# Optimization experiments

Hardware: AMD Instinct MI355X
Metric: run time of the kernel (lower is better)

The kernel has to match this reference:

```python
import jax, jax.numpy as jnp
import numpy as np

K = 20
EPS = 1e-5
SLOPE = 0.2


def knn(x, k=K):
    # x: (B, C, N); returns indices of k nearest neighbors (largest -dist^2), (B, N, k)
    xx = jnp.sum(x * x, axis=1)                      # (B, N)
    inner = jnp.einsum('bcn,bcm->bnm', x, x)         # (B, N, N)
    pd = 2.0 * inner - xx[:, :, None] - xx[:, None, :]  # -squared distance
    _, idx = jax.lax.top_k(pd, k)
    return idx


def graph_feature(x, idx):
    # x: (B, C, N), idx: (B, N, k) -> (B, 2C, N): concat(x, max_k(neighbor) - x)
    feat = jnp.transpose(x, (0, 2, 1))               # (B, N, C)
    nb = jax.vmap(lambda f, i: f[i])(feat, idx)      # (B, N, k, C)
    nb_max = nb.max(axis=2)                          # (B, N, C)
    out = jnp.concatenate([feat, nb_max - feat], axis=-1)  # (B, N, 2C)
    return jnp.transpose(out, (0, 2, 1))


def conv_bn_lrelu(x, W, g, b):
    # 1x1 Conv2d (no bias) on (B,C,N,1) == channel matmul; BN2d training-mode; LeakyReLU
    h = jnp.einsum('oc,bcn->bon', W, x)              # (B, O, N)
    mu = h.mean(axis=(0, 2), keepdims=True)
    var = h.var(axis=(0, 2), keepdims=True)
    h = (h - mu) / jnp.sqrt(var + EPS) * g[None, :, None] + b[None, :, None]
    return jax.nn.leaky_relu(h, SLOPE)


def bn1d_lrelu(h, g, b):
    mu = h.mean(axis=0, keepdims=True)
    var = h.var(axis=0, keepdims=True)
    h = (h - mu) / jnp.sqrt(var + EPS) * g[None, :] + b[None, :]
    return jax.nn.leaky_relu(h, SLOPE)


def forward(x, W1, g1, b1, W2, g2, b2, W3, g3, b3, W4, g4, b4, W5, g5, b5,
            L1, g6, b6, L2, bl2, g7, b7, L3, bl3):
    B = x.shape[0]
    idx = knn(x)                                      # knn on raw xyz
    h = conv_bn_lrelu(x, W1, g1, b1)                  # (B, 64, N)
    x1 = graph_feature(h, idx)                        # (B, 128, N)

    idx = knn(x1)
    h = conv_bn_lrelu(x1, W2, g2, b2)                 # (B, 64, N)
    x2 = graph_feature(h, idx)                        # (B, 128, N)

    idx = knn(x2)
    h = conv_bn_lrelu(x2, W3, g3, b3)                 # (B, 64, N)
    x3 = graph_feature(h, idx)                        # (B, 128, N)

    idx = knn(x3)
    h = conv_bn_lrelu(x3, W4, g4, b4)                 # (B, 128, N)
    x4 = graph_feature(h, idx)                        # (B, 256, N)

    xc = jnp.concatenate([x1, x2, x3, x4], axis=1)    # (B, 640, N)
    h5 = conv_bn_lrelu(xc, W5, g5, b5)                # (B, 1024, N)
    feat = h5.max(axis=1)                             # max over CHANNELS -> (B, N=1024)

    h = bn1d_lrelu(feat @ L1.T, g6, b6)               # (B, 512); dropout=identity (eval)
    h = bn1d_lrelu(h @ L2.T + bl2, g7, b7)            # (B, 256)
    return h @ L3.T + bl3                             # (B, 40)


def setup_inputs() -> dict:
    key = jax.random.key(0)
    ks = jax.random.split(key, 32)
    ki = iter(ks)

    def rn(shape, scale=0.1):
        return jax.random.normal(next(ki), shape, dtype=jnp.float32) * scale

    def bn_params(c):
        return 1.0 + rn((c,)), rn((c,))

    x = jax.random.normal(next(ki), (32, 3, 1024), dtype=jnp.float32)
    W1 = rn((64, 3));    g1, b1 = bn_params(64)
    W2 = rn((64, 128));  g2, b2 = bn_params(64)
    W3 = rn((64, 128));  g3, b3 = bn_params(64)
    W4 = rn((128, 128)); g4, b4 = bn_params(128)
    W5 = rn((1024, 640)); g5, b5 = bn_params(1024)
    L1 = rn((512, 1024)); g6, b6 = bn_params(512)
    L2 = rn((256, 512)); bl2 = rn((256,)); g7, b7 = bn_params(256)
    L3 = rn((40, 256));  bl3 = rn((40,))
    return dict(x=x, W1=W1, g1=g1, b1=b1, W2=W2, g2=g2, b2=b2, W3=W3, g3=g3, b3=b3,
                W4=W4, g4=g4, b4=b4, W5=W5, g5=g5, b5=b5, L1=L1, g6=g6, b6=b6,
                L2=L2, bl2=bl2, g7=g7, b7=b7, L3=L3, bl3=bl3)


def reference(x, W1, g1, b1, W2, g2, b2, W3, g3, b3, W4, g4, b4, W5, g5, b5,
              L1, g6, b6, L2, bl2, g7, b7, L3, bl3):
    return forward(x, W1, g1, b1, W2, g2, b2, W3, g3, b3, W4, g4, b4, W5, g5, b5,
                   L1, g6, b6, L2, bl2, g7, b7, L3, bl3)
```

## Files before the change

kernel.cpp:

```cpp
#include <hip/hip_runtime.h>
#include <cfloat>
#include <cstdint>

#define NB 32
#define NPTS 1024
#define KNN 20
#define RTOT (NB * NPTS)

typedef __attribute__((ext_vector_type(8))) short bf16x8;
typedef __attribute__((ext_vector_type(4))) float f32x4;

__device__ __forceinline__ float lrelu(float v) { return v >= 0.f ? v : 0.2f * v; }

__global__ void k_transpose_x(const float* __restrict__ x, float* __restrict__ xT) {
    int g = blockIdx.x * 256 + threadIdx.x;
    if (g >= NB * 3 * NPTS) return;
    int n = g % NPTS;
    int c = (g / NPTS) % 3;
    int b = g / (3 * NPTS);
    xT[((size_t)b * NPTS + n) * 3 + c] = x[g];
}

__global__ void k_xx(const float* __restrict__ X, int ldx, int C, float* __restrict__ xx) {
    int r = blockIdx.x * 256 + threadIdx.x;
    if (r >= RTOT) return;
    const float* p = X + (size_t)r * ldx;
    float s = 0.f;
    for (int c = 0; c < C; ++c) { float v = p[c]; s += v * v; }
    xx[r] = s;
}

__global__ __launch_bounds__(256) void k_gemm_xwt(
    const float* __restrict__ X, int ldx, int K,
    const float* __restrict__ W,
    float* __restrict__ H, int ldh)
{
    __shared__ float As[16][68];
    __shared__ float Bs[16][68];
    int tid = threadIdx.x;
    int tx = tid & 15, ty = tid >> 4;
    int c0 = blockIdx.x * 64;
    int r0 = blockIdx.y * 64;
    float acc[4][4] = {};
    int lr = tid >> 4, lk = tid & 15;
    for (int k0 = 0; k0 < K; k0 += 16) {
#pragma unroll
        for (int i = 0; i < 4; ++i) {
            int row = lr + i * 16;
            int kk = k0 + lk;
            float av = 0.f, bv = 0.f;
            if (kk < K) {
                av = X[(size_t)(r0 + row) * ldx + kk];
                bv = W[(size_t)(c0 + row) * K + kk];
            }
            As[lk][row] = av;
            Bs[lk][row] = bv;
        }
        __syncthreads();
#pragma unroll
        for (int k = 0; k < 16; ++k) {
            float4 a4 = *(const float4*)&As[k][ty * 4];
            float4 b4 = *(const float4*)&Bs[k][tx * 4];
            float av[4] = {a4.x, a4.y, a4.z, a4.w};
            float bv[4] = {b4.x, b4.y, b4.z, b4.w};
#pragma unroll
            for (int i = 0; i < 4; ++i)
#pragma unroll
                for (int j = 0; j < 4; ++j)
                    acc[i][j] = fmaf(av[i], bv[j], acc[i][j]);
        }
        __syncthreads();
    }
#pragma unroll
    for (int i = 0; i < 4; ++i) {
        float4 v = make_float4(acc[i][0], acc[i][1], acc[i][2], acc[i][3]);
        *(float4*)&H[(size_t)(r0 + ty * 4 + i) * ldh + c0 + tx * 4] = v;
    }
}

__global__ __launch_bounds__(256) void k_pd128(
    const float* __restrict__ X, int ldx, int K,
    const float* __restrict__ xx, float* __restrict__ pd)
{
    __shared__ float As[16][132];
    __shared__ float Bs[16][132];
    int b = blockIdx.z;
    int tid = threadIdx.x;
    int tx = tid & 15, ty = tid >> 4;
    int c0 = blockIdx.x * 128;
    int r0 = blockIdx.y * 128;
    const float* Xb = X + (size_t)b * NPTS * ldx;
    int lk = tid & 15, lr = tid >> 4;
    float acc[8][8] = {};
    for (int k0 = 0; k0 < K; k0 += 16) {
#pragma unroll
        for (int i = 0; i < 8; ++i) {
            int row = lr + i * 16;
            int kk = k0 + lk;
            float av = 0.f, bv = 0.f;
            if (kk < K) {
                av = Xb[(size_t)(r0 + row) * ldx + kk];
                bv = Xb[(size_t)(c0 + row) * ldx + kk];
            }
            As[lk][row] = av;
            Bs[lk][row] = bv;
        }
        __syncthreads();
#pragma unroll
        for (int k = 0; k < 16; ++k) {
            float a[8], bb[8];
            *(float4*)&a[0]  = *(const float4*)&As[k][ty * 4];
            *(float4*)&a[4]  = *(const float4*)&As[k][64 + ty * 4];
            *(float4*)&bb[0] = *(const float4*)&Bs[k][tx * 4];
            *(float4*)&bb[4] = *(const float4*)&Bs[k][64 + tx * 4];
#pragma unroll
            for (int i = 0; i < 8; ++i)
#pragma unroll
                for (int j = 0; j < 8; ++j)
                    acc[i][j] = fmaf(a[i], bb[j], acc[i][j]);
        }
        __syncthreads();
    }
    const float* xxb = xx + (size_t)b * NPTS;
    float* pdb = pd + (size_t)b * NPTS * NPTS;
    float xcA[4], xcB[4];
#pragma unroll
    for (int j = 0; j < 4; ++j) {
        xcA[j] = xxb[c0 + tx * 4 + j];
        xcB[j] = xxb[c0 + 64 + tx * 4 + j];
    }
#pragma unroll
    for (int i = 0; i < 8; ++i) {
        int r = r0 + ((i < 4) ? (ty * 4 + i) : (64 + ty * 4 + i - 4));
        float xr = xxb[r];
        float* orow = &pdb[(size_t)r * NPTS + c0];
        float4 v0, v1;
        v0.x = 2.f * acc[i][0] - xr - xcA[0];
        v0.y = 2.f * acc[i][1] - xr - xcA[1];
        v0.z = 2.f * acc[i][2] - xr - xcA[2];
        v0.w = 2.f * acc[i][3] - xr - xcA[3];
        v1.x = 2.f * acc[i][4] - xr - xcB[0];
        v1.y = 2.f * acc[i][5] - xr - xcB[1];
        v1.z = 2.f * acc[i][6] - xr - xcB[2];
        v1.w = 2.f * acc[i][7] - xr - xcB[3];
        *(float4*)&orow[tx * 4]      = v0;
        *(float4*)&orow[64 + tx * 4] = v1;
    }
}

__global__ __launch_bounds__(256) void k_topk_wave(const float* __restrict__ pd, int* __restrict__ idx) {
    int wid = (blockIdx.x * 256 + threadIdx.x) >> 6;
    int lane = threadIdx.x & 63;
    const float* row = pd + (size_t)wid * NPTS;
    float v[16];
#pragma unroll
    for (int j = 0; j < 16; ++j) v[j] = row[lane + 64 * j];
    float bv = v[0]; int bj = 0;
#pragma unroll
    for (int j = 1; j < 16; ++j) if (v[j] > bv) { bv = v[j]; bj = j; }
    int* out = idx + (size_t)wid * KNN;
    for (int kk = 0; kk < KNN; ++kk) {
        float cv = bv;
        int ci = lane + (bj << 6);
#pragma unroll
        for (int s = 1; s < 64; s <<= 1) {
            float ov = __shfl_xor(cv, s);
            int oi = __shfl_xor(ci, s);
            if (ov > cv || (ov == cv && oi < ci)) { cv = ov; ci = oi; }
        }
        if (lane == 0) out[kk] = ci;
        bool mine = (ci & 63) == lane;
        int jdead = ci >> 6;
#pragma unroll
        for (int j = 0; j < 16; ++j) if (mine && j == jdead) v[j] = -FLT_MAX;
        bv = v[0]; bj = 0;
#pragma unroll
        for (int j = 1; j < 16; ++j) if (v[j] > bv) { bv = v[j]; bj = j; }
    }
}

__device__ __forceinline__ void split2(float x, ushort& h, ushort& l) {
    uint u = __float_as_uint(x);
    uint r = u + 0x7FFFu + ((u >> 16) & 1u);
    ushort hh = (ushort)(r >> 16);
    float hf = __uint_as_float((uint)hh << 16);
    float d = x - hf;
    uint u2 = __float_as_uint(d);
    uint r2 = u2 + 0x7FFFu + ((u2 >> 16) & 1u);
    h = hh;
    l = (ushort)(r2 >> 16);
}

__device__ __forceinline__ uint pack2(ushort a, ushort b) { return (uint)a | ((uint)b << 16); }

__device__ __forceinline__ void stage_split(const float* __restrict__ g,
                                            ushort* __restrict__ dh, ushort* __restrict__ dl) {
    float4 v0 = *(const float4*)(g);
    float4 v1 = *(const float4*)(g + 4);
    float4 v2 = *(const float4*)(g + 8);
    float4 v3 = *(const float4*)(g + 12);
    float xs[16] = {v0.x, v0.y, v0.z, v0.w, v1.x, v1.y, v1.z, v1.w,
                    v2.x, v2.y, v2.z, v2.w, v3.x, v3.y, v3.z, v3.w};
    ushort h[16], l[16];
#pragma unroll
    for (int i = 0; i < 16; ++i) split2(xs[i], h[i], l[i]);
    uint4 H0, H1, L0, L1;
    H0.x = pack2(h[0], h[1]);  H0.y = pack2(h[2], h[3]);
    H0.z = pack2(h[4], h[5]);  H0.w = pack2(h[6], h[7]);
    H1.x = pack2(h[8], h[9]);  H1.y = pack2(h[10], h[11]);
    H1.z = pack2(h[12], h[13]); H1.w = pack2(h[14], h[15]);
    L0.x = pack2(l[0], l[1]);  L0.y = pack2(l[2], l[3]);
    L0.z = pack2(l[4], l[5]);  L0.w = pack2(l[6], l[7]);
    L1.x = pack2(l[8], l[9]);  L1.y = pack2(l[10], l[11]);
    L1.z = pack2(l[12], l[13]); L1.w = pack2(l[14], l[15]);
    *(uint4*)(dh)     = H0;
    *(uint4*)(dh + 8) = H1;
    *(uint4*)(dl)     = L0;
    *(uint4*)(dl + 8) = L1;
}

__global__ void k_split(const float* __restrict__ X, ushort* __restrict__ Xh,
                        ushort* __restrict__ Xl, int n) {
    int g = (blockIdx.x * 256 + threadIdx.x) * 8;
    if (g >= n) return;
    float4 a = *(const float4*)(X + g);
    float4 b = *(const float4*)(X + g + 4);
    float xs[8] = {a.x, a.y, a.z, a.w, b.x, b.y, b.z, b.w};
    ushort h[8], l[8];
#pragma unroll
    for (int i = 0; i < 8; ++i) split2(xs[i], h[i], l[i]);
    uint4 H, L;
    H.x = pack2(h[0], h[1]); H.y = pack2(h[2], h[3]);
    H.z = pack2(h[4], h[5]); H.w = pack2(h[6], h[7]);
    L.x = pack2(l[0], l[1]); L.y = pack2(l[2], l[3]);
    L.z = pack2(l[4], l[5]); L.w = pack2(l[6], l[7]);
    *(uint4*)(Xh + g) = H;
    *(uint4*)(Xl + g) = L;
}

#define LDK 40
__global__ __launch_bounds__(256) void k_gemm5_mfma(
    const float* __restrict__ X, const ushort* __restrict__ Wh, const ushort* __restrict__ Wl,
    float* __restrict__ H, float* __restrict__ sums)
{
    __shared__ __align__(16) ushort sAh[128 * LDK];
    __shared__ __align__(16) ushort sAl[128 * LDK];
    __shared__ __align__(16) ushort sBh[128 * LDK];
    __shared__ __align__(16) ushort sBl[128 * LDK];
    int tid = threadIdx.x;
    int lane = tid & 63, w = tid >> 6;
    int wm = w >> 1, wn = w & 1;
    int bid = blockIdx.x;
    int wg = (bid & 7) * 256 + (bid >> 3);
    int cb = wg & 7, rb = wg >> 3;
    int r0 = rb * 128, c0 = cb * 128;
    int srow = tid >> 1, sk = (tid & 1) * 16;
    int fr = lane & 15;
    int kg = (lane >> 4) << 3;
    f32x4 acc[4][4] = {};
    for (int k0 = 0; k0 < 640; k0 += 32) {
        stage_split(X + (size_t)(r0 + srow) * 640 + k0 + sk,
                    &sAh[srow * LDK + sk], &sAl[srow * LDK + sk]);
        {
            size_t gb = (size_t)(c0 + srow) * 640 + k0 + sk;
            *(uint4*)&sBh[srow * LDK + sk]     = *(const uint4*)(Wh + gb);
            *(uint4*)&sBh[srow * LDK + sk + 8] = *(const uint4*)(Wh + gb + 8);
            *(uint4*)&sBl[srow * LDK + sk]     = *(const uint4*)(Wl + gb);
            *(uint4*)&sBl[srow * LDK + sk + 8] = *(const uint4*)(Wl + gb + 8);
        }
        __syncthreads();
        bf16x8 ah[4], al[4];
#pragma unroll
        for (int mi = 0; mi < 4; ++mi) {
            int rr = wm * 64 + mi * 16 + fr;
            ah[mi] = *(const bf16x8*)&sAh[rr * LDK + kg];
            al[mi] = *(const bf16x8*)&sAl[rr * LDK + kg];
        }
#pragma unroll
        for (int ni = 0; ni < 4; ++ni) {
            int cc = wn * 64 + ni * 16 + fr;
            bf16x8 bh = *(const bf16x8*)&sBh[cc * LDK + kg];
            bf16x8 bl = *(const bf16x8*)&sBl[cc * LDK + kg];
#pragma unroll
            for (int mi = 0; mi < 4; ++mi) {
                acc[mi][ni] = __builtin_amdgcn_mfma_f32_16x16x32_bf16(ah[mi], bh, acc[mi][ni], 0, 0, 0);
                acc[mi][ni] = __builtin_amdgcn_mfma_f32_16x16x32_bf16(ah[mi], bl, acc[mi][ni], 0, 0, 0);
                acc[mi][ni] = __builtin_amdgcn_mfma_f32_16x16x32_bf16(al[mi], bh, acc[mi][ni], 0, 0, 0);
            }
        }
        __syncthreads();
    }
#pragma unroll
    for (int mi = 0; mi < 4; ++mi) {
        int rg = r0 + wm * 64 + mi * 16 + (lane >> 4) * 4;
#pragma unroll
        for (int ni = 0; ni < 4; ++ni) {
            int cg = c0 + wn * 64 + ni * 16 + fr;
#pragma unroll
            for (int r = 0; r < 4; ++r)
                H[(size_t)(rg + r) * 1024 + cg] = acc[mi][ni][r];
        }
    }
    float* csum  = (float*)sAh;
    float* csum2 = csum + 128;
    if (tid < 128) { csum[tid] = 0.f; csum2[tid] = 0.f; }
    __syncthreads();
#pragma unroll
    for (int ni = 0; ni < 4; ++ni) {
        float s = 0.f, s2 = 0.f;
#pragma unroll
        for (int mi = 0; mi < 4; ++mi)
#pragma unroll
            for (int r = 0; r < 4; ++r) { float v = acc[mi][ni][r]; s += v; s2 += v * v; }
        int c = wn * 64 + ni * 16 + fr;
        atomicAdd(&csum[c], s);
        atomicAdd(&csum2[c], s2);
    }
    __syncthreads();
    if (tid < 128) {
        atomicAdd(&sums[c0 + tid], csum[tid]);
        atomicAdd(&sums[1024 + c0 + tid], csum2[tid]);
    }
}

__global__ __launch_bounds__(256) void k_bn_stats(const float* __restrict__ H, int ldh, int O, int R,
                                                  float* __restrict__ sums) {
    int nblk = gridDim.x;
    int rows = (R + nblk - 1) / nblk;
    int r0 = blockIdx.x * rows;
    int r1 = r0 + rows; if (r1 > R) r1 = R;
    int tid = threadIdx.x;
    if (O <= 256) {
        int per = 256 / O;
        int c = tid % O;
        int rOff = tid / O;
        float s = 0.f, s2 = 0.f;
        for (int r = r0 + rOff; r < r1; r += per) {
            float v = H[(size_t)r * ldh + c];
            s += v; s2 += v * v;
        }
        __shared__ float ls[256], ls2[256];
        ls[tid] = s; ls2[tid] = s2;
        __syncthreads();
        for (int st = 128; st >= O; st >>= 1) {
            if (tid < st) { ls[tid] += ls[tid + st]; ls2[tid] += ls2[tid + st]; }
            __syncthreads();
        }
        if (tid < O) {
            atomicAdd(&sums[c], ls[tid]);
            atomicAdd(&sums[O + c], ls2[tid]);
        }
    } else {
        int nc = O / 256;
        float s[4] = {0, 0, 0, 0}, s2[4] = {0, 0, 0, 0};
        for (int r = r0; r < r1; ++r) {
            const float* rowp = H + (size_t)r * ldh;
            for (int i = 0; i < nc; ++i) {
                float v = rowp[tid + i * 256];
                s[i] += v; s2[i] += v * v;
            }
        }
        for (int i = 0; i < nc; ++i) {
            atomicAdd(&sums[tid + i * 256], s[i]);
            atomicAdd(&sums[O + tid + i * 256], s2[i]);
        }
    }
}

__global__ void k_bn_finalize(const float* __restrict__ sums, const float* __restrict__ g,
                              const float* __restrict__ bta, int O, float invR,
                              float* __restrict__ ss) {
    int o = blockIdx.x * 256 + threadIdx.x;
    if (o >= O) return;
    float mu = sums[o] * invR;
    float var = sums[O + o] * invR - mu * mu;
    float sc = g[o] / sqrtf(var + 1e-5f);
    ss[o] = sc;
    ss[O + o] = bta[o] - mu * sc;
}

__global__ __launch_bounds__(256) void k_graph_feature(
    const float* __restrict__ hT, int ldh, int C,
    const int* __restrict__ idx, const float* __restrict__ ss,
    float* __restrict__ out, int ldo, int colOff)
{
    int ppb = 256 / C;
    int p = threadIdx.x / C;
    int c = threadIdx.x % C;
    int r = blockIdx.x * ppb + p;
    int b = r >> 10;
    float sc = ss[c], sh = ss[C + c];
    float self = hT[(size_t)r * ldh + c];
    float vs = lrelu(sc * self + sh);
    const int* ip = idx + (size_t)r * KNN;
    float m = -FLT_MAX;
#pragma unroll 4
    for (int k = 0; k < KNN; ++k) {
        int j = ip[k];
        float hv = hT[((size_t)b * NPTS + j) * ldh + c];
        float v = lrelu(sc * hv + sh);
        m = fmaxf(m, v);
    }
    float* orow = out + (size_t)r * ldo + colOff;
    orow[c] = vs;
    orow[C + c] = m - vs;
}

__global__ __launch_bounds__(256) void k_chanmax(const float* __restrict__ h5,
                                                 const float* __restrict__ ss,
                                                 float* __restrict__ feat) {
    int r = blockIdx.x;
    int tid = threadIdx.x;
    __shared__ float red[256];
    const float* rowp = h5 + (size_t)r * 1024;
    float m = -FLT_MAX;
    for (int o = tid; o < 1024; o += 256) {
        float v = lrelu(ss[o] * rowp[o] + ss[1024 + o]);
        m = fmaxf(m, v);
    }
    red[tid] = m;
    __syncthreads();
    for (int s = 128; s > 0; s >>= 1) {
        if (tid < s) red[tid] = fmaxf(red[tid], red[tid + s]);
        __syncthreads();
    }
    if (tid == 0) feat[r] = red[0];
}

__global__ void k_fc(const float* __restrict__ in, const float* __restrict__ Lw,
                     const float* __restrict__ bias, float* __restrict__ out, int K, int J) {
    int g = blockIdx.x * 256 + threadIdx.x;
    if (g >= 32 * J) return;
    int b = g / J, j = g % J;
    const float* xr = in + (size_t)b * K;
    const float* wr = Lw + (size_t)j * K;
    float acc = 0.f;
    for (int k = 0; k < K; ++k) acc = fmaf(xr[k], wr[k], acc);
    out[g] = bias ? acc + bias[j] : acc;
}

__global__ void k_bn1d(float* __restrict__ h, const float* __restrict__ g,
                       const float* __restrict__ bta, int J) {
    int j = blockIdx.x * 256 + threadIdx.x;
    if (j >= J) return;
    float s = 0.f, s2 = 0.f;
    for (int b = 0; b < 32; ++b) {
        float v = h[b * J + j];
        s += v; s2 += v * v;
    }
    float mu = s / 32.f;
    float var = s2 / 32.f - mu * mu;
    float sc = g[j] / sqrtf(var + 1e-5f);
    float sh = bta[j] - mu * sc;
    for (int b = 0; b < 32; ++b) {
        float v = sc * h[b * J + j] + sh;
        h[b * J + j] = lrelu(v);
    }
}

extern "C" void kernel_launch(void* const* d_in, const int* in_sizes, int n_in,
                              void* d_out, int out_size, void* d_ws, size_t ws_size,
                              hipStream_t stream) {
    const float* x   = (const float*)d_in[0];
    const float* W1  = (const float*)d_in[1];
    const float* g1  = (const float*)d_in[2];
    const float* b1  = (const float*)d_in[3];
    const float* W2  = (const float*)d_in[4];
    const float* g2  = (const float*)d_in[5];
    const float* b2  = (const float*)d_in[6];
    const float* W3  = (const float*)d_in[7];
    const float* g3  = (const float*)d_in[8];
    const float* b3  = (const float*)d_in[9];
    const float* W4  = (const float*)d_in[10];
    const float* g4  = (const float*)d_in[11];
    const float* b4  = (const float*)d_in[12];
    const float* W5  = (const float*)d_in[13];
    const float* g5  = (const float*)d_in[14];
    const float* b5  = (const float*)d_in[15];
    const float* L1  = (const float*)d_in[16];
    const float* g6  = (const float*)d_in[17];
    const float* b6  = (const float*)d_in[18];
    const float* L2  = (const float*)d_in[19];
    const float* bl2 = (const float*)d_in[20];
    const float* g7  = (const float*)d_in[21];
    const float* b7  = (const float*)d_in[22];
    const float* L3  = (const float*)d_in[23];
    const float* bl3 = (const float*)d_in[24];

    float* ws = (float*)d_ws;
    size_t off = 0;
    auto alloc = [&](size_t n) { size_t o = off; off += (n + 63) & ~(size_t)63; return o; };
    float* pd   = ws + alloc((size_t)NB * NPTS * NPTS);
    float* h5   = pd;
    float* xcT  = ws + alloc((size_t)RTOT * 640);
    float* hbuf = ws + alloc((size_t)RTOT * 128);
    float* xT   = ws + alloc((size_t)RTOT * 3);
    float* xxb  = ws + alloc(RTOT);
    float* sums = ws + alloc(2048);
    float* ss   = ws + alloc(2048);
    float* feat = ws + alloc(RTOT);
    float* h1   = ws + alloc(32 * 512);
    float* h2   = ws + alloc(32 * 256);
    int*   idxb = (int*)(ws + alloc((size_t)RTOT * KNN));
    ushort* W5h = (ushort*)(ws + alloc(1024 * 640 / 2));
    ushort* W5l = (ushort*)(ws + alloc(1024 * 640 / 2));

    k_transpose_x<<<(NB * 3 * NPTS + 255) / 256, 256, 0, stream>>>(x, xT);
    k_split<<<(1024 * 640 / 8 + 255) / 256, 256, 0, stream>>>(W5, W5h, W5l, 1024 * 640);

    auto run_knn = [&](const float* X, int ldx, int C) {
        k_xx<<<(RTOT + 255) / 256, 256, 0, stream>>>(X, ldx, C, xxb);
        k_pd128<<<dim3(NPTS / 128, NPTS / 128, NB), 256, 0, stream>>>(X, ldx, C, xxb, pd);
        k_topk_wave<<<RTOT / 4, 256, 0, stream>>>(pd, idxb);
    };
    auto run_conv = [&](const float* X, int ldx, int K, const float* W,
                        const float* g, const float* bta, int O) {
        k_gemm_xwt<<<dim3(O / 64, RTOT / 64), 256, 0, stream>>>(X, ldx, K, W, hbuf, O);
        hipMemsetAsync(sums, 0, 2 * O * sizeof(float), stream);
        k_bn_stats<<<256, 256, 0, stream>>>(hbuf, O, O, RTOT, sums);
        k_bn_finalize<<<(O + 255) / 256, 256, 0, stream>>>(sums, g, bta, O, 1.f / RTOT, ss);
    };
    auto run_gf = [&](int C, int colOff) {
        int ppb = 256 / C;
        k_graph_feature<<<RTOT / ppb, 256, 0, stream>>>(hbuf, C, C, idxb, ss, xcT, 640, colOff);
    };

    run_knn(xT, 3, 3);
    run_conv(xT, 3, 3, W1, g1, b1, 64);
    run_gf(64, 0);

    run_knn(xcT + 0, 640, 128);
    run_conv(xcT + 0, 640, 128, W2, g2, b2, 64);
    run_gf(64, 128);

    run_knn(xcT + 128, 640, 128);
    run_conv(xcT + 128, 640, 128, W3, g3, b3, 64);
    run_gf(64, 256);

    run_knn(xcT + 256, 640, 128);
    run_conv(xcT + 256, 640, 128, W4, g4, b4, 128);
    run_gf(128, 384);

    hipMemsetAsync(sums, 0, 2048 * sizeof(float), stream);
    k_gemm5_mfma<<<2048, 256, 0, stream>>>(xcT, W5h, W5l, h5, sums);
    k_bn_finalize<<<4, 256, 0, stream>>>(sums, g5, b5, 1024, 1.f / RTOT, ss);
    k_chanmax<<<RTOT, 256, 0, stream>>>(h5, ss, feat);

    k_fc<<<(32 * 512 + 255) / 256, 256, 0, stream>>>(feat, L1, nullptr, h1, 1024, 512);
    k_bn1d<<<(512 + 255) / 256, 256, 0, stream>>>(h1, g6, b6, 512);
    k_fc<<<(32 * 256 + 255) / 256, 256, 0, stream>>>(h1, L2, bl2, h2, 512, 256);
    k_bn1d<<<(256 + 255) / 256, 256, 0, stream>>>(h2, g7, b7, 256);
    k_fc<<<(32 * 40 + 255) / 256, 256, 0, stream>>>(h2, L3, bl3, (float*)d_out, 256, 40);
}
```

Before: 1.828 ms.

## Exploit pairwise-distance symmetry: compute upper-triangle tiles and mirror-write transposes

The pairwise distance kernel now launches only the 36 upper-triangular 128x128 tiles per batch, not all 64. Each off-diagonal tile writes both its own block and the transposed block, roughly halving the GEMM work for the distance matrix. The feature dimension also becomes a template parameter so the K loop can be unrolled or specialized. The transposed writes are strided across rows and less coalesced, and fewer blocks means lower parallelism per launch.

```diff
diff --git a/kernel.cpp b/kernel.cpp
--- a/kernel.cpp
+++ b/kernel.cpp
@@ -78,17 +78,20 @@
     }
 }
 
-__global__ __launch_bounds__(256) void k_pd128(
-    const float* __restrict__ X, int ldx, int K,
+template<int K>
+__global__ __launch_bounds__(256) void k_pd_sym(
+    const float* __restrict__ X, int ldx,
     const float* __restrict__ xx, float* __restrict__ pd)
 {
     __shared__ float As[16][132];
     __shared__ float Bs[16][132];
-    int b = blockIdx.z;
+    int b = blockIdx.y;
     int tid = threadIdx.x;
     int tx = tid & 15, ty = tid >> 4;
-    int c0 = blockIdx.x * 128;
-    int r0 = blockIdx.y * 128;
+    int t = blockIdx.x, rb = 0, rem = 8;
+    while (t >= rem) { t -= rem; ++rb; --rem; }
+    int cb = rb + t;
+    int r0 = rb * 128, c0 = cb * 128;
     const float* Xb = X + (size_t)b * NPTS * ldx;
     int lk = tid & 15, lr = tid >> 4;
     float acc[8][8] = {};
@@ -123,28 +126,47 @@
     }
     const float* xxb = xx + (size_t)b * NPTS;
     float* pdb = pd + (size_t)b * NPTS * NPTS;
-    float xcA[4], xcB[4];
-#pragma unroll
-    for (int j = 0; j < 4; ++j) {
-        xcA[j] = xxb[c0 + tx * 4 + j];
-        xcB[j] = xxb[c0 + 64 + tx * 4 + j];
-    }
+    float xc[8];
+#pragma unroll
+    for (int j = 0; j < 8; ++j)
+        xc[j] = xxb[c0 + ((j < 4) ? (tx * 4 + j) : (64 + tx * 4 + j - 4))];
+    float xr[8];
+#pragma unroll
+    for (int i = 0; i < 8; ++i)
+        xr[i] = xxb[r0 + ((i < 4) ? (ty * 4 + i) : (64 + ty * 4 + i - 4))];
 #pragma unroll
     for (int i = 0; i < 8; ++i) {
         int r = r0 + ((i < 4) ? (ty * 4 + i) : (64 + ty * 4 + i - 4));
-        float xr = xxb[r];
         float* orow = &pdb[(size_t)r * NPTS + c0];
         float4 v0, v1;
-        v0.x = 2.f * acc[i][0] - xr - xcA[0];
-        v0.y = 2.f * acc[i][1] - xr - xcA[1];
-        v0.z = 2.f * acc[i][2] - xr - xcA[2];
-        v0.w = 2.f * acc[i][3] - xr - xcA[3];
-        v1.x = 2.f * acc[i][4] - xr - xcB[0];
-        v1.y = 2.f * acc[i][5] - xr - xcB[1];
-        v1.z = 2.f * acc[i][6] - xr - xcB[2];
-        v1.w = 2.f * acc[i][7] - xr - xcB[3];
+        v0.x = 2.f * acc[i][0] - xr[i] - xc[0];
+        v0.y = 2.f * acc[i][1] - xr[i] - xc[1];
+        v0.z = 2.f * acc[i][2] - xr[i] - xc[2];
+        v0.w = 2.f * acc[i][3] - xr[i] - xc[3];
+        v1.x = 2.f * acc[i][4] - xr[i] - xc[4];
+        v1.y = 2.f * acc[i][5] - xr[i] - xc[5];
+        v1.z = 2.f * acc[i][6] - xr[i] - xc[6];
+        v1.w = 2.f * acc[i][7] - xr[i] - xc[7];
         *(float4*)&orow[tx * 4]      = v0;
         *(float4*)&orow[64 + tx * 4] = v1;
+    }
+    if (cb > rb) {
+#pragma unroll
+        for (int j = 0; j < 8; ++j) {
+            int c = c0 + ((j < 4) ? (tx * 4 + j) : (64 + tx * 4 + j - 4));
+            float* orow = &pdb[(size_t)c * NPTS + r0];
+            float4 w0, w1;
+            w0.x = 2.f * acc[0][j] - xc[j] - xr[0];
+            w0.y = 2.f * acc[1][j] - xc[j] - xr[1];
+            w0.z = 2.f * acc[2][j] - xc[j] - xr[2];
+            w0.w = 2.f * acc[3][j] - xc[j] - xr[3];
+            w1.x = 2.f * acc[4][j] - xc[j] - xr[4];
+            w1.y = 2.f * acc[5][j] - xc[j] - xr[5];
+            w1.z = 2.f * acc[6][j] - xc[j] - xr[6];
+            w1.w = 2.f * acc[7][j] - xc[j] - xr[7];
+            *(float4*)&orow[ty * 4]      = w0;
+            *(float4*)&orow[64 + ty * 4] = w1;
+        }
     }
 }
 
@@ -510,7 +532,10 @@
 
     auto run_knn = [&](const float* X, int ldx, int C) {
         k_xx<<<(RTOT + 255) / 256, 256, 0, stream>>>(X, ldx, C, xxb);
-        k_pd128<<<dim3(NPTS / 128, NPTS / 128, NB), 256, 0, stream>>>(X, ldx, C, xxb, pd);
+        if (C == 3)
+            k_pd_sym<3><<<dim3(36, NB), 256, 0, stream>>>(X, ldx, xxb, pd);
+        else
+            k_pd_sym<128><<<dim3(36, NB), 256, 0, stream>>>(X, ldx, xxb, pd);
         k_topk_wave<<<RTOT / 4, 256, 0, stream>>>(pd, idxb);
     };
     auto run_conv = [&](const float* X, int ldx, int K, const float* W,
```

Measured after the change: 1.678 ms. 1.09x faster.
